# Kernel tuning notes

Hardware: AMD Instinct MI355X
Metric: run time of the kernel (lower is better)

Reference implementation:

```python
import jax, jax.numpy as jnp
import numpy as np

NEG_SLOPE = 0.2  # PyG GATConv default leaky_relu negative_slope


def gat_conv(x, edge_index, W, att_src, att_dst, bias, heads, out_ch):
    """PyG GATConv (add_self_loops=False, concat=True, dropout disabled)."""
    N = x.shape[0]
    src, dst = edge_index[0], edge_index[1]
    h = (x @ W).reshape(N, heads, out_ch)               # [N,H,C]
    a_src = jnp.einsum('nhc,hc->nh', h, att_src)        # [N,H]
    a_dst = jnp.einsum('nhc,hc->nh', h, att_dst)        # [N,H]
    e = jax.nn.leaky_relu(a_src[src] + a_dst[dst], NEG_SLOPE)  # [E,H]
    # segment softmax over edges grouped by destination node
    e_max = jax.ops.segment_max(e, dst, num_segments=N)  # [N,H]
    e_exp = jnp.exp(e - e_max[dst])
    denom = jax.ops.segment_sum(e_exp, dst, num_segments=N)
    alpha = e_exp / (denom[dst] + 1e-16)                 # [E,H]
    msg = h[src] * alpha[:, :, None]                     # [E,H,C]
    out = jax.ops.segment_sum(msg, dst, num_segments=N)  # [N,H,C]
    return out.reshape(N, heads * out_ch) + bias


def setup_inputs() -> dict:
    key = jax.random.key(0)
    ks = jax.random.split(key, 10)
    N, E, F_IN, H, C1, OUT = 50000, 1600000, 256, 8, 8, 64
    s = 0.1
    return {
        'x': jax.random.normal(ks[0], (N, F_IN), jnp.float32),
        'edge_index': jax.random.randint(ks[1], (2, E), 0, N, jnp.int64),
        'W1': jax.random.normal(ks[2], (F_IN, H * C1), jnp.float32) * s,
        'att_src1': jax.random.normal(ks[3], (H, C1), jnp.float32) * s,
        'att_dst1': jax.random.normal(ks[4], (H, C1), jnp.float32) * s,
        'bias1': jax.random.normal(ks[5], (H * C1,), jnp.float32) * s,
        'W2': jax.random.normal(ks[6], (H * C1, OUT), jnp.float32) * s,
        'att_src2': jax.random.normal(ks[7], (1, OUT), jnp.float32) * s,
        'att_dst2': jax.random.normal(ks[8], (1, OUT), jnp.float32) * s,
        'bias2': jax.random.normal(ks[9], (OUT,), jnp.float32) * s,
    }


def reference(x, edge_index, W1, att_src1, att_dst1, bias1, W2, att_src2, att_dst2, bias2):
    # GAT.forward, eval mode with disable_dropout=True (no dropout, no loss)
    h = gat_conv(x, edge_index, W1, att_src1, att_dst1, bias1, heads=8, out_ch=8)
    h = jax.nn.elu(h)
    h = gat_conv(h, edge_index, W2, att_src2, att_dst2, bias2, heads=1, out_ch=64)
    return jax.nn.log_softmax(h, axis=1)
```

## Files before the change

### kernel.cpp

```cpp
#include <hip/hip_runtime.h>
#include <math.h>

#define LRELU 0.2f
#define BSH 5
#define BSZ (1 << BSH)
#define CH 8192
#define GB 10
#define CAP 1408
#define NBMAX 1600

typedef __attribute__((ext_vector_type(8))) short bf16x8;
typedef __attribute__((ext_vector_type(4))) float f32x4;

static __device__ __forceinline__ float bf2f(unsigned int u16) {
    union { unsigned int i; float f; } c; c.i = u16 << 16; return c.f;
}
static __device__ __forceinline__ unsigned short f2bf(float f) {
    union { float f; unsigned int i; } c; c.f = f;
    unsigned int x = c.i;
    return (unsigned short)((x + 0x7fffu + ((x >> 16) & 1u)) >> 16);
}


__global__ __launch_bounds__(256) void k_prep(const float* __restrict__ W1,
                                              const float* __restrict__ W2,
                                              const float* __restrict__ as2in,
                                              const float* __restrict__ ad2in,
                                              unsigned short* __restrict__ Wt1,
                                              unsigned short* __restrict__ Wt2,
                                              unsigned short* __restrict__ h1b,
                                              unsigned short* __restrict__ gb,
                                              float* __restrict__ w2s,
                                              float* __restrict__ w2d,
                                              int* __restrict__ bcur,
                                              int N, int NB) {
    int idx = blockIdx.x * 256 + threadIdx.x;
    if (idx < 16384) {
        int n = idx >> 8, k = idx & 255;
        Wt1[idx] = f2bf(W1[k * 64 + n]);
    } else if (idx < 16384 + 4096) {
        int j = idx - 16384;
        int n = j >> 6, k = j & 63;
        Wt2[j] = f2bf(W2[k * 64 + n]);
    } else if (idx >= 20480 && idx < 20544) {
        h1b[(size_t)N * 64 + (idx - 20480)] = 0;
    } else if (idx >= 20544 && idx < 20608) {
        gb[(size_t)N * 64 + (idx - 20544)] = 0;
    } else if (idx >= 20608 && idx < 20672) {
        int c = idx - 20608;
        float s = 0.f;
#pragma unroll
        for (int n = 0; n < 64; ++n) s += W2[c * 64 + n] * as2in[n];
        w2s[c] = s;
    } else if (idx >= 20672 && idx < 20736) {
        int c = idx - 20672;
        float s = 0.f;
#pragma unroll
        for (int n = 0; n < 64; ++n) s += W2[c * 64 + n] * ad2in[n];
        w2d[c] = s;
    } else if (idx >= 20736 && idx < 20736 + NB) {
        int b = idx - 20736;
        bcur[b] = b * CAP;
    }
}


__global__ __launch_bounds__(256) void k_mid(const int* __restrict__ src,
                                             const int* __restrict__ dstArr,
                                             int E, int NB,
                                             int* __restrict__ bcur,
                                             unsigned* __restrict__ pairs,
                                             const float* __restrict__ X,
                                             const unsigned short* __restrict__ Wt,
                                             const float* __restrict__ attd,
                                             int N, unsigned short* __restrict__ Hb,
                                             float* __restrict__ adst,
                                             int nchunk) {
    __shared__ short Xl[64 * 256];
    __shared__ int cnt2[NBMAX];
    int t = threadIdx.x;
    if ((int)blockIdx.x < nchunk) {
        int* lds_d = (int*)Xl;
        int e0 = blockIdx.x * CH;
        int e1 = e0 + CH; if (e1 > E) e1 = E;
        int n = e1 - e0;
        for (int b = t; b < NBMAX; b += 256) cnt2[b] = 0;
        __syncthreads();
        for (int i = t; i < n; i += 256) {
            int d = dstArr[e0 + i];
            lds_d[i] = d;
            atomicAdd(&cnt2[d >> BSH], 1);
        }
        __syncthreads();
        for (int b = t; b < NB; b += 256) {
            int c = cnt2[b];
            cnt2[b] = c ? atomicAdd(&bcur[b], c) : 0;
        }
        __syncthreads();
        for (int i = t; i < n; i += 256) {
            int d = lds_d[i];
            int p = atomicAdd(&cnt2[d >> BSH], 1);
            pairs[p] = ((unsigned)src[e0 + i] << BSH) | (unsigned)(d & (BSZ - 1));
        }
        return;
    }
    int bx = (int)blockIdx.x - nchunk;
    int l = t & 63, w = t >> 6;
    int rblk = bx * 64;

    int half = l >> 5;
    int c8 = (l & 31) * 8;
#pragma unroll
    for (int i = 0; i < 8; ++i) {
        int rl = w * 16 + i * 2 + half;
        int row = rblk + rl;
        float4 x0 = {0.f, 0.f, 0.f, 0.f}, x1 = {0.f, 0.f, 0.f, 0.f};
        if (row < N) {
            x0 = *reinterpret_cast<const float4*>(X + (size_t)row * 256 + c8);
            x1 = *reinterpret_cast<const float4*>(X + (size_t)row * 256 + c8 + 4);
        }
        bf16x8 p;
        p[0] = (short)f2bf(x0.x); p[1] = (short)f2bf(x0.y);
        p[2] = (short)f2bf(x0.z); p[3] = (short)f2bf(x0.w);
        p[4] = (short)f2bf(x1.x); p[5] = (short)f2bf(x1.y);
        p[6] = (short)f2bf(x1.z); p[7] = (short)f2bf(x1.w);
        int g = (l & 31) ^ (rl & 7);
        *reinterpret_cast<bf16x8*>(&Xl[rl * 256 + g * 8]) = p;
    }
    __syncthreads();

    int m = l & 15, quad = l >> 4;
    int rl = w * 16 + m;
    f32x4 acc0 = {0.f, 0.f, 0.f, 0.f}, acc1 = acc0, acc2 = acc0, acc3 = acc0;
#pragma unroll
    for (int tt = 0; tt < 8; ++tt) {
        int g = (tt * 4 + quad) ^ (m & 7);
        bf16x8 a = *reinterpret_cast<const bf16x8*>(&Xl[rl * 256 + g * 8]);
        int kk = tt * 32 + quad * 8;
        bf16x8 b0 = *reinterpret_cast<const bf16x8*>(&Wt[(0 * 16 + m) * 256 + kk]);
        bf16x8 b1 = *reinterpret_cast<const bf16x8*>(&Wt[(1 * 16 + m) * 256 + kk]);
        bf16x8 b2 = *reinterpret_cast<const bf16x8*>(&Wt[(2 * 16 + m) * 256 + kk]);
        bf16x8 b3 = *reinterpret_cast<const bf16x8*>(&Wt[(3 * 16 + m) * 256 + kk]);
        acc0 = __builtin_amdgcn_mfma_f32_16x16x32_bf16(a, b0, acc0, 0, 0, 0);
        acc1 = __builtin_amdgcn_mfma_f32_16x16x32_bf16(a, b1, acc1, 0, 0, 0);
        acc2 = __builtin_amdgcn_mfma_f32_16x16x32_bf16(a, b2, acc2, 0, 0, 0);
        acc3 = __builtin_amdgcn_mfma_f32_16x16x32_bf16(a, b3, acc3, 0, 0, 0);
    }

    int r0 = rblk + w * 16;
    f32x4 accs[4] = {acc0, acc1, acc2, acc3};
#pragma unroll
    for (int nt = 0; nt < 4; ++nt) {
        int cn = nt * 16 + m;
        float av_d = attd[cn];
#pragma unroll
        for (int r = 0; r < 4; ++r) {
            int row = r0 + quad * 4 + r;
            float hv = accs[nt][r];
            if (row < N) Hb[(size_t)row * 64 + cn] = f2bf(hv);
            float vd = hv * av_d;
            vd += __shfl_xor(vd, 1, 64); vd += __shfl_xor(vd, 2, 64); vd += __shfl_xor(vd, 4, 64);
            if ((m & 7) == 0 && row < N) {
                adst[row * 8 + (cn >> 3)] = vd;
            }
        }
    }
}


__global__ __launch_bounds__(256) void k_gather1f(const int* __restrict__ bcur,
                                                  const unsigned* __restrict__ pairs,
                                                  const uint4* __restrict__ Hb8,
                                                  const float* __restrict__ adst,
                                                  const float* __restrict__ attS,
                                                  const float* __restrict__ bias,
                                                  const unsigned short* __restrict__ Wt2,
                                                  const float* __restrict__ w2d,
                                                  int N,
                                                  unsigned short* __restrict__ Gb,
                                                  float* __restrict__ ad2) {
    __shared__ int pairsS[CAP];
    __shared__ int colT[CAP];
    __shared__ int cntS[BSZ];
    __shared__ int baseS[BSZ];
    __shared__ int curS[BSZ];
    __shared__ short h2l[32 * 64];
    int t = threadIdx.x;
    int gid = t >> 3, sub = t & 7;
    int b = blockIdx.x;
    int d0 = b << BSH;
    int d = d0 + gid;
    int dok = (d < N);
    int dc = dok ? d : d0;
    float adv = dok ? adst[dc * 8 + sub] : 0.f;
    float aS[8];
#pragma unroll
    for (int c = 0; c < 8; ++c) aS[c] = attS[sub * 8 + c];

    int jb = b * CAP;
    int n = bcur[b] - jb;
    if (t < BSZ) cntS[t] = 0;
    __syncthreads();
    for (int i = t; i < n; i += 256) {
        int pk = (int)pairs[jb + i];
        pairsS[i] = pk;
        atomicAdd(&cntS[pk & (BSZ - 1)], 1);
    }
    __syncthreads();
    if (t < 64) {
        int v = (t < BSZ) ? cntS[t] : 0;
        int inc = v;
#pragma unroll
        for (int off = 1; off < BSZ; off <<= 1) {
            int q = __shfl_up(inc, off, 64);
            if (t >= off) inc += q;
        }
        if (t < BSZ) { baseS[t] = inc - v; curS[t] = inc - v; }
    }
    __syncthreads();
    for (int i = t; i < n; i += 256) {
        int pk = pairsS[i];
        int p = atomicAdd(&curS[pk & (BSZ - 1)], 1);
        colT[p] = pk >> BSH;
    }
    __syncthreads();

    int lo = baseS[gid];
    int hi = lo + cntS[gid];

    float acc[8] = {0.f, 0.f, 0.f, 0.f, 0.f, 0.f, 0.f, 0.f};
    float denom = 0.f;
    for (int u = lo; u < hi; u += GB) {
        uint4 hv8[GB];
#pragma unroll
        for (int q = 0; q < GB; ++q) {
            int uu = u + q;
            int s = (uu < hi) ? colT[uu] : N;
            hv8[q] = Hb8[(size_t)s * 8 + sub];
        }
        __builtin_amdgcn_sched_barrier(0);
#pragma unroll
        for (int q = 0; q < GB; ++q) {
            uint4 hv = hv8[q];
            float f0 = bf2f(hv.x & 0xffffu), f1 = bf2f(hv.x >> 16);
            float f2 = bf2f(hv.y & 0xffffu), f3 = bf2f(hv.y >> 16);
            float f4 = bf2f(hv.z & 0xffffu), f5 = bf2f(hv.z >> 16);
            float f6 = bf2f(hv.w & 0xffffu), f7 = bf2f(hv.w >> 16);
            float ps = f0 * aS[0];
            ps = fmaf(f1, aS[1], ps); ps = fmaf(f2, aS[2], ps);
            ps = fmaf(f3, aS[3], ps); ps = fmaf(f4, aS[4], ps);
            ps = fmaf(f5, aS[5], ps); ps = fmaf(f6, aS[6], ps);
            ps = fmaf(f7, aS[7], ps);
            float e = ps + adv;
            e = (e > 0.f) ? e : LRELU * e;
            float wgt = ((u + q) < hi) ? __expf(e) : 0.f;
            denom += wgt;
            acc[0] = fmaf(wgt, f0, acc[0]); acc[1] = fmaf(wgt, f1, acc[1]);
            acc[2] = fmaf(wgt, f2, acc[2]); acc[3] = fmaf(wgt, f3, acc[3]);
            acc[4] = fmaf(wgt, f4, acc[4]); acc[5] = fmaf(wgt, f5, acc[5]);
            acc[6] = fmaf(wgt, f6, acc[6]); acc[7] = fmaf(wgt, f7, acc[7]);
        }
    }

    float invd = 1.f / (denom + 1e-16f);
    float v[8];
#pragma unroll
    for (int c = 0; c < 8; ++c) {
        float x = fmaf(acc[c], invd, bias[sub * 8 + c]);
        v[c] = (x > 0.f) ? x : expm1f(x);
    }
    float vd = 0.f;
#pragma unroll
    for (int c = 0; c < 8; ++c) vd = fmaf(v[c], w2d[sub * 8 + c], vd);
    vd += __shfl_xor(vd, 1, 64); vd += __shfl_xor(vd, 2, 64); vd += __shfl_xor(vd, 4, 64);
    if (dok && sub == 0) ad2[d] = vd;

    bf16x8 p;
#pragma unroll
    for (int c = 0; c < 8; ++c) p[c] = (short)f2bf(v[c]);
    *reinterpret_cast<bf16x8*>(&h2l[gid * 64 + (sub ^ (gid & 7)) * 8]) = p;
    __syncthreads();

    int l = t & 63, w = t >> 6;
    int m = l & 15, quad = l >> 4;
    int mt = w & 1;
    int ntb = (w >> 1) * 2;
    int r = mt * 16 + m;
    f32x4 g0 = {0.f, 0.f, 0.f, 0.f}, g1 = g0;
#pragma unroll
    for (int tt = 0; tt < 2; ++tt) {
        bf16x8 a = *reinterpret_cast<const bf16x8*>(
            &h2l[r * 64 + ((tt * 4 + quad) ^ (r & 7)) * 8]);
        int kk = tt * 32 + quad * 8;
        bf16x8 b0 = *reinterpret_cast<const bf16x8*>(&Wt2[((ntb + 0) * 16 + m) * 64 + kk]);
        bf16x8 b1 = *reinterpret_cast<const bf16x8*>(&Wt2[((ntb + 1) * 16 + m) * 64 + kk]);
        g0 = __builtin_amdgcn_mfma_f32_16x16x32_bf16(a, b0, g0, 0, 0, 0);
        g1 = __builtin_amdgcn_mfma_f32_16x16x32_bf16(a, b1, g1, 0, 0, 0);
    }
    f32x4 gs[2] = {g0, g1};
#pragma unroll
    for (int nt = 0; nt < 2; ++nt) {
        int cn = (ntb + nt) * 16 + m;
#pragma unroll
        for (int rr = 0; rr < 4; ++rr) {
            int dr = d0 + mt * 16 + quad * 4 + rr;
            if (dr < N) Gb[(size_t)dr * 64 + cn] = f2bf(gs[nt][rr]);
        }
    }
}


__global__ __launch_bounds__(256) void k_gather2(const int* __restrict__ bcur,
                                                 const unsigned* __restrict__ pairs,
                                                 const uint4* __restrict__ Gb8,
                                                 const float* __restrict__ adst,
                                                 const float* __restrict__ w2s,
                                                 const float* __restrict__ bias,
                                                 int N,
                                                 float* __restrict__ out) {
    __shared__ int pairsS[CAP];
    __shared__ int colT[CAP];
    __shared__ int cntS[BSZ];
    __shared__ int baseS[BSZ];
    __shared__ int curS[BSZ];
    int t = threadIdx.x;
    int gid = t >> 3, sub = t & 7;
    int b = blockIdx.x;
    int d0 = b << BSH;
    int d = d0 + gid;
    int dok = (d < N);
    int dc = dok ? d : d0;
    float adv = dok ? adst[dc] : 0.f;
    float wS[8];
#pragma unroll
    for (int c = 0; c < 8; ++c) wS[c] = w2s[sub * 8 + c];

    int jb = b * CAP;
    int n = bcur[b] - jb;
    if (t < BSZ) cntS[t] = 0;
    __syncthreads();
    for (int i = t; i < n; i += 256) {
        int pk = (int)pairs[jb + i];
        pairsS[i] = pk;
        atomicAdd(&cntS[pk & (BSZ - 1)], 1);
    }
    __syncthreads();
    if (t < 64) {
        int v = (t < BSZ) ? cntS[t] : 0;
        int inc = v;
#pragma unroll
        for (int off = 1; off < BSZ; off <<= 1) {
            int q = __shfl_up(inc, off, 64);
            if (t >= off) inc += q;
        }
        if (t < BSZ) { baseS[t] = inc - v; curS[t] = inc - v; }
    }
    __syncthreads();
    for (int i = t; i < n; i += 256) {
        int pk = pairsS[i];
        int p = atomicAdd(&curS[pk & (BSZ - 1)], 1);
        colT[p] = pk >> BSH;
    }
    __syncthreads();

    int lo = baseS[gid];
    int hi = lo + cntS[gid];

    float acc[8] = {0.f, 0.f, 0.f, 0.f, 0.f, 0.f, 0.f, 0.f};
    float denom = 0.f;
    for (int u = lo; u < hi; u += GB) {
        uint4 hv8[GB];
#pragma unroll
        for (int q = 0; q < GB; ++q) {
            int uu = u + q;
            int s = (uu < hi) ? colT[uu] : N;
            hv8[q] = Gb8[(size_t)s * 8 + sub];
        }
        __builtin_amdgcn_sched_barrier(0);
#pragma unroll
        for (int q = 0; q < GB; ++q) {
            uint4 hv = hv8[q];
            float f0 = bf2f(hv.x & 0xffffu), f1 = bf2f(hv.x >> 16);
            float f2 = bf2f(hv.y & 0xffffu), f3 = bf2f(hv.y >> 16);
            float f4 = bf2f(hv.z & 0xffffu), f5 = bf2f(hv.z >> 16);
            float f6 = bf2f(hv.w & 0xffffu), f7 = bf2f(hv.w >> 16);
            float ps = f0 * wS[0];
            ps = fmaf(f1, wS[1], ps); ps = fmaf(f2, wS[2], ps);
            ps = fmaf(f3, wS[3], ps); ps = fmaf(f4, wS[4], ps);
            ps = fmaf(f5, wS[5], ps); ps = fmaf(f6, wS[6], ps);
            ps = fmaf(f7, wS[7], ps);
            ps += __shfl_xor(ps, 1, 64);
            ps += __shfl_xor(ps, 2, 64);
            ps += __shfl_xor(ps, 4, 64);
            float e = ps + adv;
            e = (e > 0.f) ? e : LRELU * e;
            float wgt = ((u + q) < hi) ? __expf(e) : 0.f;
            denom += wgt;
            acc[0] = fmaf(wgt, f0, acc[0]); acc[1] = fmaf(wgt, f1, acc[1]);
            acc[2] = fmaf(wgt, f2, acc[2]); acc[3] = fmaf(wgt, f3, acc[3]);
            acc[4] = fmaf(wgt, f4, acc[4]); acc[5] = fmaf(wgt, f5, acc[5]);
            acc[6] = fmaf(wgt, f6, acc[6]); acc[7] = fmaf(wgt, f7, acc[7]);
        }
    }
    float invd = 1.f / (denom + 1e-16f);
    float v[8];
#pragma unroll
    for (int c = 0; c < 8; ++c) v[c] = fmaf(acc[c], invd, bias[sub * 8 + c]);
    float m = v[0];
#pragma unroll
    for (int c = 1; c < 8; ++c) m = fmaxf(m, v[c]);
    m = fmaxf(m, __shfl_xor(m, 1, 64));
    m = fmaxf(m, __shfl_xor(m, 2, 64));
    m = fmaxf(m, __shfl_xor(m, 4, 64));
    float se = 0.f;
#pragma unroll
    for (int c = 0; c < 8; ++c) se += __expf(v[c] - m);
    se += __shfl_xor(se, 1, 64);
    se += __shfl_xor(se, 2, 64);
    se += __shfl_xor(se, 4, 64);
    float ls = m + __logf(se);
    if (dok) {
        float4 o0, o1;
        o0.x = v[0] - ls; o0.y = v[1] - ls; o0.z = v[2] - ls; o0.w = v[3] - ls;
        o1.x = v[4] - ls; o1.y = v[5] - ls; o1.z = v[6] - ls; o1.w = v[7] - ls;
        *reinterpret_cast<float4*>(&out[(size_t)d * 64 + sub * 8]) = o0;
        *reinterpret_cast<float4*>(&out[(size_t)d * 64 + sub * 8 + 4]) = o1;
    }
}


extern "C" void kernel_launch(void* const* d_in, const int* in_sizes, int n_in,
                              void* d_out, int out_size, void* d_ws, size_t ws_size,
                              hipStream_t stream) {
    const float* x   = (const float*)d_in[0];
    const int*   ei  = (const int*)d_in[1];
    const float* W1  = (const float*)d_in[2];
    const float* as1 = (const float*)d_in[3];
    const float* ad1 = (const float*)d_in[4];
    const float* b1  = (const float*)d_in[5];
    const float* W2  = (const float*)d_in[6];
    const float* as2 = (const float*)d_in[7];
    const float* ad2 = (const float*)d_in[8];
    const float* b2  = (const float*)d_in[9];
    float* out = (float*)d_out;

    const int N = in_sizes[0] / 256;
    const int E = in_sizes[1] / 2;
    const int* src = ei;
    const int* dst = ei + E;
    const int NB = (N + BSZ - 1) >> BSH;
    const int nchunk = (E + CH - 1) / CH;

    char* ws = (char*)d_ws;
    size_t off = 0;
    auto alloc = [&](size_t bytes) -> void* {
        void* p = ws + off;
        off = (off + bytes + 255) & ~(size_t)255;
        return p;
    };
    int*      bcur   = (int*)alloc((size_t)NB * 4);
    unsigned* pairs  = (unsigned*)alloc((size_t)NB * CAP * 4);
    unsigned short* wt1 = (unsigned short*)alloc(64 * 256 * 2);
    unsigned short* wt2 = (unsigned short*)alloc(64 * 64 * 2);
    unsigned short* h1b = (unsigned short*)alloc((size_t)(N + 1) * 64 * 2);
    float* a_d1   = (float*)alloc((size_t)N * 8 * 4);
    unsigned short* gb  = (unsigned short*)alloc((size_t)(N + 1) * 64 * 2);
    float* a_d2   = (float*)alloc((size_t)N * 4);
    float* w2s    = (float*)alloc(64 * 4);
    float* w2d    = (float*)alloc(64 * 4);
    (void)ws_size; (void)n_in; (void)out_size;

    int prep_blocks = (20736 + NB + 255) / 256;
    k_prep<<<prep_blocks, 256, 0, stream>>>(W1, W2, as2, ad2, wt1, wt2,
                                            h1b, gb, w2s, w2d, bcur, N, NB);

    int gblk = (N + 63) / 64;
    k_mid<<<nchunk + gblk, 256, 0, stream>>>(src, dst, E, NB, bcur, pairs,
                                             x, wt1, ad1, N, h1b, a_d1, nchunk);

    k_gather1f<<<NB, 256, 0, stream>>>(bcur, pairs, (const uint4*)h1b,
                                       a_d1, as1, b1, wt2, w2d,
                                       N, gb, a_d2);

    k_gather2<<<NB, 256, 0, stream>>>(bcur, pairs, (const uint4*)gb,
                                      a_d2, w2s, b2, N, out);
}
```

Baseline: 224.6 us.

## Bucket edges by 128-node coarse buckets and filter per 32-node gather block

The edge scatter now bins edges into coarse buckets of 128 destination nodes instead of 32. This cuts the LDS counter array in the scatter blocks and the number of global atomic reservations per chunk. Each gather block covering 32 destinations scans its whole coarse bucket twice from global memory and keeps only its quarter. That removes the pairsS staging buffer but reads and filters about four times as many pair entries per block. Larger buckets with CAPC 4608 also make the fixed-capacity layout less sensitive to degree skew.

Result: slower. 253.4 us (+12.8%).

```diff
diff --git a/kernel.cpp b/kernel.cpp
--- a/kernel.cpp
+++ b/kernel.cpp
@@ -2,12 +2,13 @@
 #include <math.h>
 
 #define LRELU 0.2f
-#define BSH 5
-#define BSZ (1 << BSH)
+#define CBSH 7
+#define CBSZ (1 << CBSH)
+#define CAPC 4608
+#define GDS 32
 #define CH 8192
 #define GB 10
-#define CAP 1408
-#define NBMAX 1600
+#define CAPG 1408
 
 typedef __attribute__((ext_vector_type(8))) short bf16x8;
 typedef __attribute__((ext_vector_type(4))) float f32x4;
@@ -33,7 +34,7 @@
                                               float* __restrict__ w2s,
                                               float* __restrict__ w2d,
                                               int* __restrict__ bcur,
-                                              int N, int NB) {
+                                              int N, int NBC) {
     int idx = blockIdx.x * 256 + threadIdx.x;
     if (idx < 16384) {
         int n = idx >> 8, k = idx & 255;
@@ -58,16 +59,16 @@
 #pragma unroll
         for (int n = 0; n < 64; ++n) s += W2[c * 64 + n] * ad2in[n];
         w2d[c] = s;
-    } else if (idx >= 20736 && idx < 20736 + NB) {
+    } else if (idx >= 20736 && idx < 20736 + NBC) {
         int b = idx - 20736;
-        bcur[b] = b * CAP;
+        bcur[b] = b * CAPC;
     }
 }
 
 
 __global__ __launch_bounds__(256) void k_mid(const int* __restrict__ src,
                                              const int* __restrict__ dstArr,
-                                             int E, int NB,
+                                             int E, int NBC,
                                              int* __restrict__ bcur,
                                              unsigned* __restrict__ pairs,
                                              const float* __restrict__ X,
@@ -77,30 +78,30 @@
                                              float* __restrict__ adst,
                                              int nchunk) {
     __shared__ short Xl[64 * 256];
-    __shared__ int cnt2[NBMAX];
+    __shared__ int cnt2[512];
     int t = threadIdx.x;
     if ((int)blockIdx.x < nchunk) {
         int* lds_d = (int*)Xl;
         int e0 = blockIdx.x * CH;
         int e1 = e0 + CH; if (e1 > E) e1 = E;
         int n = e1 - e0;
-        for (int b = t; b < NBMAX; b += 256) cnt2[b] = 0;
+        for (int b = t; b < 512; b += 256) cnt2[b] = 0;
         __syncthreads();
         for (int i = t; i < n; i += 256) {
             int d = dstArr[e0 + i];
             lds_d[i] = d;
-            atomicAdd(&cnt2[d >> BSH], 1);
+            atomicAdd(&cnt2[d >> CBSH], 1);
         }
         __syncthreads();
-        for (int b = t; b < NB; b += 256) {
+        for (int b = t; b < NBC; b += 256) {
             int c = cnt2[b];
             cnt2[b] = c ? atomicAdd(&bcur[b], c) : 0;
         }
         __syncthreads();
         for (int i = t; i < n; i += 256) {
             int d = lds_d[i];
-            int p = atomicAdd(&cnt2[d >> BSH], 1);
-            pairs[p] = ((unsigned)src[e0 + i] << BSH) | (unsigned)(d & (BSZ - 1));
+            int p = atomicAdd(&cnt2[d >> CBSH], 1);
+            pairs[p] = ((unsigned)src[e0 + i] << CBSH) | (unsigned)(d & (CBSZ - 1));
         }
         return;
     }
@@ -179,16 +180,15 @@
                                                   int N,
                                                   unsigned short* __restrict__ Gb,
                                                   float* __restrict__ ad2) {
-    __shared__ int pairsS[CAP];
-    __shared__ int colT[CAP];
-    __shared__ int cntS[BSZ];
-    __shared__ int baseS[BSZ];
-    __shared__ int curS[BSZ];
+    __shared__ int colT[CAPG];
+    __shared__ int cntS[GDS];
+    __shared__ int baseS[GDS];
+    __shared__ int curS[GDS];
     __shared__ short h2l[32 * 64];
     int t = threadIdx.x;
     int gid = t >> 3, sub = t & 7;
     int b = blockIdx.x;
-    int d0 = b << BSH;
+    int d0 = b * GDS;
     int d = d0 + gid;
     int dok = (d < N);
     int dc = dok ? d : d0;
@@ -197,31 +197,34 @@
 #pragma unroll
     for (int c = 0; c < 8; ++c) aS[c] = attS[sub * 8 + c];
 
-    int jb = b * CAP;
-    int n = bcur[b] - jb;
-    if (t < BSZ) cntS[t] = 0;
+    int cb = b >> 2;
+    unsigned qt = (unsigned)(b & 3);
+    int cbase = cb * CAPC;
+    int n = bcur[cb] - cbase;
+    if (t < GDS) cntS[t] = 0;
     __syncthreads();
     for (int i = t; i < n; i += 256) {
-        int pk = (int)pairs[jb + i];
-        pairsS[i] = pk;
-        atomicAdd(&cntS[pk & (BSZ - 1)], 1);
+        unsigned pk = pairs[cbase + i];
+        if (((pk >> 5) & 3u) == qt) atomicAdd(&cntS[pk & (GDS - 1)], 1);
     }
     __syncthreads();
     if (t < 64) {
-        int v = (t < BSZ) ? cntS[t] : 0;
+        int v = (t < GDS) ? cntS[t] : 0;
         int inc = v;
 #pragma unroll
-        for (int off = 1; off < BSZ; off <<= 1) {
+        for (int off = 1; off < GDS; off <<= 1) {
             int q = __shfl_up(inc, off, 64);
             if (t >= off) inc += q;
         }
-        if (t < BSZ) { baseS[t] = inc - v; curS[t] = inc - v; }
+        if (t < GDS) { baseS[t] = inc - v; curS[t] = inc - v; }
     }
     __syncthreads();
     for (int i = t; i < n; i += 256) {
-        int pk = pairsS[i];
-        int p = atomicAdd(&curS[pk & (BSZ - 1)], 1);
-        colT[p] = pk >> BSH;
+        unsigned pk = pairs[cbase + i];
+        if (((pk >> 5) & 3u) == qt) {
+            int p = atomicAdd(&curS[pk & (GDS - 1)], 1);
+            colT[p] = (int)(pk >> CBSH);
+        }
     }
     __syncthreads();
 
@@ -318,15 +321,14 @@
                                                  const float* __restrict__ bias,
                                                  int N,
                                                  float* __restrict__ out) {
-    __shared__ int pairsS[CAP];
-    __shared__ int colT[CAP];
-    __shared__ int cntS[BSZ];
-    __shared__ int baseS[BSZ];
-    __shared__ int curS[BSZ];
+    __shared__ int colT[CAPG];
+    __shared__ int cntS[GDS];
+    __shared__ int baseS[GDS];
+    __shared__ int curS[GDS];
     int t = threadIdx.x;
     int gid = t >> 3, sub = t & 7;
     int b = blockIdx.x;
-    int d0 = b << BSH;
+    int d0 = b * GDS;
     int d = d0 + gid;
     int dok = (d < N);
     int dc = dok ? d : d0;
@@ -335,31 +337,34 @@
 #pragma unroll
     for (int c = 0; c < 8; ++c) wS[c] = w2s[sub * 8 + c];
 
-    int jb = b * CAP;
-    int n = bcur[b] - jb;
-    if (t < BSZ) cntS[t] = 0;
+    int cb = b >> 2;
+    unsigned qt = (unsigned)(b & 3);
+    int cbase = cb * CAPC;
+    int n = bcur[cb] - cbase;
+    if (t < GDS) cntS[t] = 0;
     __syncthreads();
     for (int i = t; i < n; i += 256) {
-        int pk = (int)pairs[jb + i];
-        pairsS[i] = pk;
-        atomicAdd(&cntS[pk & (BSZ - 1)], 1);
+        unsigned pk = pairs[cbase + i];
+        if (((pk >> 5) & 3u) == qt) atomicAdd(&cntS[pk & (GDS - 1)], 1);
     }
     __syncthreads();
     if (t < 64) {
-        int v = (t < BSZ) ? cntS[t] : 0;
+        int v = (t < GDS) ? cntS[t] : 0;
         int inc = v;
 #pragma unroll
-        for (int off = 1; off < BSZ; off <<= 1) {
+        for (int off = 1; off < GDS; off <<= 1) {
             int q = __shfl_up(inc, off, 64);
             if (t >= off) inc += q;
         }
-        if (t < BSZ) { baseS[t] = inc - v; curS[t] = inc - v; }
+        if (t < GDS) { baseS[t] = inc - v; curS[t] = inc - v; }
     }
     __syncthreads();
     for (int i = t; i < n; i += 256) {
-        int pk = pairsS[i];
-        int p = atomicAdd(&curS[pk & (BSZ - 1)], 1);
-        colT[p] = pk >> BSH;
+        unsigned pk = pairs[cbase + i];
+        if (((pk >> 5) & 3u) == qt) {
+            int p = atomicAdd(&curS[pk & (GDS - 1)], 1);
+            colT[p] = (int)(pk >> CBSH);
+        }
     }
     __syncthreads();
 
@@ -448,7 +453,8 @@
     const int E = in_sizes[1] / 2;
     const int* src = ei;
     const int* dst = ei + E;
-    const int NB = (N + BSZ - 1) >> BSH;
+    const int NBC = (N + CBSZ - 1) >> CBSH;
+    const int NG  = (N + GDS - 1) / GDS;
     const int nchunk = (E + CH - 1) / CH;
 
     char* ws = (char*)d_ws;
@@ -458,8 +464,8 @@
         off = (off + bytes + 255) & ~(size_t)255;
         return p;
     };
-    int*      bcur   = (int*)alloc((size_t)NB * 4);
-    unsigned* pairs  = (unsigned*)alloc((size_t)NB * CAP * 4);
+    int*      bcur   = (int*)alloc((size_t)NBC * 4);
+    unsigned* pairs  = (unsigned*)alloc((size_t)NBC * CAPC * 4);
     unsigned short* wt1 = (unsigned short*)alloc(64 * 256 * 2);
     unsigned short* wt2 = (unsigned short*)alloc(64 * 64 * 2);
     unsigned short* h1b = (unsigned short*)alloc((size_t)(N + 1) * 64 * 2);
@@ -470,18 +476,18 @@
     float* w2d    = (float*)alloc(64 * 4);
     (void)ws_size; (void)n_in; (void)out_size;
 
-    int prep_blocks = (20736 + NB + 255) / 256;
+    int prep_blocks = (20736 + NBC + 255) / 256;
     k_prep<<<prep_blocks, 256, 0, stream>>>(W1, W2, as2, ad2, wt1, wt2,
-                                            h1b, gb, w2s, w2d, bcur, N, NB);
+                                            h1b, gb, w2s, w2d, bcur, N, NBC);
 
     int gblk = (N + 63) / 64;
-    k_mid<<<nchunk + gblk, 256, 0, stream>>>(src, dst, E, NB, bcur, pairs,
+    k_mid<<<nchunk + gblk, 256, 0, stream>>>(src, dst, E, NBC, bcur, pairs,
                                              x, wt1, ad1, N, h1b, a_d1, nchunk);
 
-    k_gather1f<<<NB, 256, 0, stream>>>(bcur, pairs, (const uint4*)h1b,
+    k_gather1f<<<NG, 256, 0, stream>>>(bcur, pairs, (const uint4*)h1b,
                                        a_d1, as1, b1, wt2, w2d,
                                        N, gb, a_d2);
 
-    k_gather2<<<NB, 256, 0, stream>>>(bcur, pairs, (const uint4*)gb,
+    k_gather2<<<NG, 256, 0, stream>>>(bcur, pairs, (const uint4*)gb,
                                       a_d2, w2s, b2, N, out);
 }
```
